# Performance work log

Measured on AMD Instinct MI355X. Metric: run time of the kernel, lower is better.

## Reference

```python
import jax, jax.numpy as jnp
import numpy as np
import math

GAIN = 6.0
FREQ = 1000.0
Q = 0.707
SAMPLE_RATE = 44100


def _peaking_coeffs():
    # torchaudio.functional.equalizer_biquad coefficients (peaking EQ)
    w0 = 2.0 * math.pi * FREQ / SAMPLE_RATE
    A = math.exp(GAIN / 40.0 * math.log(10.0))
    alpha = math.sin(w0) / (2.0 * Q)
    b0 = 1.0 + alpha * A
    b1 = -2.0 * math.cos(w0)
    b2 = 1.0 - alpha * A
    a0 = 1.0 + alpha / A
    a1 = -2.0 * math.cos(w0)
    a2 = 1.0 - alpha / A
    # normalize by a0 (lfilter semantics)
    return (np.float32(b0 / a0), np.float32(b1 / a0), np.float32(b2 / a0),
            np.float32(a1 / a0), np.float32(a2 / a0))


def setup_inputs() -> dict:
    key = jax.random.key(0)
    x = jax.random.normal(key, (8, 2, 1200000), dtype=jnp.float32)
    return {"x": x}


def _biquad(x):
    # x: [B, C, T]; direct-form-I biquad with zero initial conditions
    b0, b1, b2, a1, a2 = _peaking_coeffs()
    # FIR part, fully vectorized: f[n] = b0*x[n] + b1*x[n-1] + b2*x[n-2]
    xp = jnp.pad(x, ((0, 0), (0, 0), (2, 0)))
    f = b0 * xp[..., 2:] + b1 * xp[..., 1:-1] + b2 * xp[..., :-2]
    # IIR part via scan over time: y[n] = f[n] - a1*y[n-1] - a2*y[n-2]
    f_t = jnp.moveaxis(f, -1, 0)  # [T, B, C]
    y0 = jnp.zeros(x.shape[:-1], dtype=x.dtype)

    def step(carry, ft):
        y1, y2 = carry
        y = ft - a1 * y1 - a2 * y2
        return (y, y1), y

    _, ys = jax.lax.scan(step, (y0, y0), f_t)
    return jnp.moveaxis(ys, 0, -1)  # [B, C, T]


def reference(x):
    return _biquad(x)
```

## Files before the change

### kernel.cpp

```cpp
#include <hip/hip_runtime.h>
#include <math.h>


typedef float f32x4 __attribute__((ext_vector_type(4)));

#define T_LEN 1200000
#define NCH   16
#define L     32
#define NR    64
#define NWARM 4
#define OUT_ROWS (NR - NWARM)
#define OUT_PER_SEG (OUT_ROWS * L)
#define SEGS (T_LEN / OUT_PER_SEG)
#define WPB 4
#define NBLOCKS 1250
#define NWAVES (NBLOCKS * WPB)
#define RSTRIDE 36
#define WAVE_LDS (NR * RSTRIDE)

struct Params {
    float b0, b1, b2, a1, a2;
    float lnr, theta, inv_sinth;
    float C[6][4];
};

__device__ __forceinline__ void load_seg(f32x4 r[8], const float* __restrict__ xc,
                                         int g0, int lane)
{
    #pragma unroll
    for (int it = 0; it < 8; ++it) {
        int g = g0 + (it << 8) + (lane << 2);
        f32x4 v = {0.f, 0.f, 0.f, 0.f};
        if (g >= 0 && g < T_LEN) v = *(const f32x4*)(xc + g);
        r[it] = v;
    }
}

__device__ __forceinline__ void stage_seg(float* __restrict__ xs, const f32x4 r[8],
                                          int lane)
{
    const int row0 = lane >> 3, j = (lane & 7) << 2;
    #pragma unroll
    for (int it = 0; it < 8; ++it) {
        int row = (it << 3) + row0;
        *(f32x4*)&xs[row * RSTRIDE + j] = r[it];
    }
}

__device__ __forceinline__ void process_seg(float* __restrict__ xs,
                                            float* __restrict__ yc, int g0, int lane,
                                            const Params& P,
                                            const float c1r[4], const float c2r[4])
{
    const int base = lane * RSTRIDE;

    float x1 = 0.f, x2 = 0.f;
    if (lane > 0) {
        x1 = xs[base - RSTRIDE + 31];
        x2 = xs[base - RSTRIDE + 30];
    }
    asm volatile("" ::: "memory");

    float v1 = 0.f, v2 = 0.f;
    #pragma unroll
    for (int b = 0; b < 8; ++b) {
        f32x4 xv = *(const f32x4*)&xs[base + (b << 2)];
        f32x4 yv;
        #pragma unroll
        for (int k = 0; k < 4; ++k) {
            float xk = xv[k];
            float f  = fmaf(P.b0, xk, fmaf(P.b1, x1, P.b2 * x2));
            float t2 = fmaf(-P.a2, v2, f);
            float yk = fmaf(-P.a1, v1, t2);
            v2 = v1; v1 = yk;
            x2 = x1; x1 = xk;
            yv[k] = yk;
        }
        *(f32x4*)&xs[base + (b << 2)] = yv;
    }

    #pragma unroll
    for (int k = 0; k < 6; ++k) {
        int d = 1 << k;
        float p1 = __shfl_up(v1, d);
        float p2 = __shfl_up(v2, d);
        if (lane < d) { p1 = 0.f; p2 = 0.f; }
        float n1 = fmaf(P.C[k][0], p1, fmaf(P.C[k][1], p2, v1));
        float n2 = fmaf(P.C[k][2], p1, fmaf(P.C[k][3], p2, v2));
        v1 = n1; v2 = n2;
    }
    float e1 = __shfl_up(v1, 1);
    float e2 = __shfl_up(v2, 1);
    if (lane == 0) { e1 = 0.f; e2 = 0.f; }

    const int j0 = (lane << 2) & 31;
    #pragma unroll
    for (int it = 0; it < 8; ++it) {
        int vo = (it << 6) + lane;
        int row = NWARM + (it << 3) + (lane >> 3);
        row = row > 63 ? 63 : row;
        float al = __shfl(e1, row);
        float be = __shfl(e2, row);
        if (vo < OUT_PER_SEG / 4) {
            f32x4 yv = *(const f32x4*)&xs[row * RSTRIDE + j0];
            f32x4 o;
            #pragma unroll
            for (int k = 0; k < 4; ++k)
                o[k] = fmaf(al, c1r[k], fmaf(be, c2r[k], yv[k]));
            int q = (vo << 2) + NWARM * L;
            __builtin_nontemporal_store(o, (f32x4*)(yc + g0 + q));
        }
    }
}

__global__ __launch_bounds__(256, 4) void eq_kernel(const float* __restrict__ x,
                                                    float* __restrict__ y, Params P)
{
    __shared__ __align__(16) float lds[WPB * WAVE_LDS];
    const int lane = threadIdx.x & 63;
    const int wid  = threadIdx.x >> 6;
    float* xs = lds + wid * WAVE_LDS;
    const int w = blockIdx.x * WPB + wid;

    float c1r[4], c2r[4];
    {
        const int t0 = (lane << 2) & 31;
        float ph[5];
        #pragma unroll
        for (int k = 0; k < 5; ++k) {
            int t = t0 - 1 + k;
            ph[k] = (t < 0) ? 0.f
                            : expf(t * P.lnr) * sinf((t + 1) * P.theta) * P.inv_sinth;
        }
        #pragma unroll
        for (int k = 0; k < 4; ++k) {
            c1r[k] = fmaf(-P.a1, ph[k + 1], -P.a2 * ph[k]);
            c2r[k] = -P.a2 * ph[k + 1];
        }
    }

    const int sA = w, sB = w + NWAVES;
    const int chA = sA / SEGS, segA = sA - chA * SEGS;
    const int chB = sB / SEGS, segB = sB - chB * SEGS;
    const int g0A = segA * OUT_PER_SEG - NWARM * L;
    const int g0B = segB * OUT_PER_SEG - NWARM * L;
    const float* xcA = x + (size_t)chA * T_LEN;
    const float* xcB = x + (size_t)chB * T_LEN;
    float* ycA = y + (size_t)chA * T_LEN;
    float* ycB = y + (size_t)chB * T_LEN;

    f32x4 ra[8], rb[8];
    load_seg(ra, xcA, g0A, lane);
    load_seg(rb, xcB, g0B, lane);
    stage_seg(xs, ra, lane);
    asm volatile("" ::: "memory");
    process_seg(xs, ycA, g0A, lane, P, c1r, c2r);
    stage_seg(xs, rb, lane);
    asm volatile("" ::: "memory");
    process_seg(xs, ycB, g0B, lane, P, c1r, c2r);
}

extern "C" void kernel_launch(void* const* d_in, const int* in_sizes, int n_in,
                              void* d_out, int out_size, void* d_ws, size_t ws_size,
                              hipStream_t stream) {
    const float* x = (const float*)d_in[0];
    float* y = (float*)d_out;

    double w0    = 2.0 * M_PI * 1000.0 / 44100.0;
    double A     = exp(6.0 / 40.0 * log(10.0));
    double al    = sin(w0) / (2.0 * 0.707);
    double b0 = 1.0 + al * A;
    double b1 = -2.0 * cos(w0);
    double b2 = 1.0 - al * A;
    double a0 = 1.0 + al / A;
    double a1 = -2.0 * cos(w0);
    double a2 = 1.0 - al / A;
    b0 /= a0; b1 /= a0; b2 /= a0; a1 /= a0; a2 /= a0;

    Params P;
    P.b0 = (float)b0; P.b1 = (float)b1; P.b2 = (float)b2;
    P.a1 = (float)a1; P.a2 = (float)a2;

    double r     = sqrt(a2);
    double theta = acos(-a1 / (2.0 * r));
    P.lnr = (float)log(r);
    P.theta = (float)theta;
    P.inv_sinth = (float)(1.0 / sin(theta));

    double m00 = -a1, m01 = -a2, m10 = 1.0, m11 = 0.0;
    for (int s = 0; s < 5; ++s) {
        double t00 = m00 * m00 + m01 * m10;
        double t01 = m00 * m01 + m01 * m11;
        double t10 = m10 * m00 + m11 * m10;
        double t11 = m10 * m01 + m11 * m11;
        m00 = t00; m01 = t01; m10 = t10; m11 = t11;
    }
    for (int k = 0; k < 6; ++k) {
        P.C[k][0] = (float)m00; P.C[k][1] = (float)m01;
        P.C[k][2] = (float)m10; P.C[k][3] = (float)m11;
        double t00 = m00 * m00 + m01 * m10;
        double t01 = m00 * m01 + m01 * m11;
        double t10 = m10 * m00 + m11 * m10;
        double t11 = m10 * m01 + m11 * m11;
        m00 = t00; m01 = t01; m10 = t10; m11 = t11;
    }

    eq_kernel<<<NBLOCKS, 256, 0, stream>>>(x, y, P);
}
```

Measured before the change: 29.53 us.

## Use persistent-style waves processing 4-5 segments with double-buffered register prefetch

Cuts the grid from 1250 to 512 blocks, so each wave handles four or five segments instead of two. Each next segment's global loads are issued into registers before the current segment is processed, overlapping memory latency with the scan compute. Launch bounds drop to 2 blocks per SIMD, which lowers occupancy and leaves latency hiding to the software prefetch. This also raises per-wave serial work and the tail imbalance from the conditional fifth segment.

```diff
diff --git a/kernel.cpp b/kernel.cpp
--- a/kernel.cpp
+++ b/kernel.cpp
@@ -11,9 +11,10 @@
 #define NWARM 4
 #define OUT_ROWS (NR - NWARM)
 #define OUT_PER_SEG (OUT_ROWS * L)
-#define SEGS (T_LEN / OUT_PER_SEG)
+#define SEGS_PER_CH (T_LEN / OUT_PER_SEG)
+#define NSEG (SEGS_PER_CH * NCH)
 #define WPB 4
-#define NBLOCKS 1250
+#define NBLOCKS 512
 #define NWAVES (NBLOCKS * WPB)
 #define RSTRIDE 36
 #define WAVE_LDS (NR * RSTRIDE)
@@ -24,14 +25,27 @@
     float C[6][4];
 };
 
-__device__ __forceinline__ void load_seg(f32x4 r[8], const float* __restrict__ xc,
-                                         int g0, int lane)
+struct Seg { const float* xc; float* yc; int g0; };
+
+__device__ __forceinline__ Seg mkseg(int s, const float* __restrict__ x,
+                                     float* __restrict__ y)
+{
+    int ch = s / SEGS_PER_CH;
+    int si = s - ch * SEGS_PER_CH;
+    Seg g;
+    g.xc = x + (size_t)ch * T_LEN;
+    g.yc = y + (size_t)ch * T_LEN;
+    g.g0 = si * OUT_PER_SEG - NWARM * L;
+    return g;
+}
+
+__device__ __forceinline__ void load_seg(f32x4 r[8], const Seg& s, int lane)
 {
     #pragma unroll
     for (int it = 0; it < 8; ++it) {
-        int g = g0 + (it << 8) + (lane << 2);
+        int g = s.g0 + (it << 8) + (lane << 2);
         f32x4 v = {0.f, 0.f, 0.f, 0.f};
-        if (g >= 0 && g < T_LEN) v = *(const f32x4*)(xc + g);
+        if (g >= 0 && g < T_LEN) v = *(const f32x4*)(s.xc + g);
         r[it] = v;
     }
 }
@@ -48,7 +62,7 @@
 }
 
 __device__ __forceinline__ void process_seg(float* __restrict__ xs,
-                                            float* __restrict__ yc, int g0, int lane,
+                                            const Seg& s, int lane,
                                             const Params& P,
                                             const float c1r[4], const float c2r[4])
 {
@@ -108,12 +122,14 @@
             for (int k = 0; k < 4; ++k)
                 o[k] = fmaf(al, c1r[k], fmaf(be, c2r[k], yv[k]));
             int q = (vo << 2) + NWARM * L;
-            __builtin_nontemporal_store(o, (f32x4*)(yc + g0 + q));
-        }
-    }
-}
-
-__global__ __launch_bounds__(256, 4) void eq_kernel(const float* __restrict__ x,
+            __builtin_nontemporal_store(o, (f32x4*)(s.yc + s.g0 + q));
+        }
+    }
+}
+
+#define MEMBAR asm volatile("" ::: "memory")
+
+__global__ __launch_bounds__(256, 2) void eq_kernel(const float* __restrict__ x,
                                                     float* __restrict__ y, Params P)
 {
     __shared__ __align__(16) float lds[WPB * WAVE_LDS];
@@ -139,25 +155,36 @@
         }
     }
 
-    const int sA = w, sB = w + NWAVES;
-    const int chA = sA / SEGS, segA = sA - chA * SEGS;
-    const int chB = sB / SEGS, segB = sB - chB * SEGS;
-    const int g0A = segA * OUT_PER_SEG - NWARM * L;
-    const int g0B = segB * OUT_PER_SEG - NWARM * L;
-    const float* xcA = x + (size_t)chA * T_LEN;
-    const float* xcB = x + (size_t)chB * T_LEN;
-    float* ycA = y + (size_t)chA * T_LEN;
-    float* ycB = y + (size_t)chB * T_LEN;
+    const Seg s0 = mkseg(w,              x, y);
+    const Seg s1 = mkseg(w + NWAVES,     x, y);
+    const Seg s2 = mkseg(w + 2 * NWAVES, x, y);
+    const Seg s3 = mkseg(w + 3 * NWAVES, x, y);
+    const bool has4 = (w + 4 * NWAVES) < NSEG;
+    const Seg s4 = mkseg(has4 ? (w + 4 * NWAVES) : w, x, y);
 
     f32x4 ra[8], rb[8];
-    load_seg(ra, xcA, g0A, lane);
-    load_seg(rb, xcB, g0B, lane);
-    stage_seg(xs, ra, lane);
-    asm volatile("" ::: "memory");
-    process_seg(xs, ycA, g0A, lane, P, c1r, c2r);
-    stage_seg(xs, rb, lane);
-    asm volatile("" ::: "memory");
-    process_seg(xs, ycB, g0B, lane, P, c1r, c2r);
+    load_seg(ra, s0, lane);
+    load_seg(rb, s1, lane);
+
+    stage_seg(xs, ra, lane); MEMBAR;
+    process_seg(xs, s0, lane, P, c1r, c2r);
+    load_seg(ra, s2, lane);
+
+    stage_seg(xs, rb, lane); MEMBAR;
+    process_seg(xs, s1, lane, P, c1r, c2r);
+    load_seg(rb, s3, lane);
+
+    stage_seg(xs, ra, lane); MEMBAR;
+    process_seg(xs, s2, lane, P, c1r, c2r);
+    if (has4) load_seg(ra, s4, lane);
+
+    stage_seg(xs, rb, lane); MEMBAR;
+    process_seg(xs, s3, lane, P, c1r, c2r);
+
+    if (has4) {
+        stage_seg(xs, ra, lane); MEMBAR;
+        process_seg(xs, s4, lane, P, c1r, c2r);
+    }
 }
 
 extern "C" void kernel_launch(void* const* d_in, const int* in_sizes, int n_in,
```

New measurement: 29.98 us. Within noise of the previous version (+1.5%).
